# Kernel optimization log

Hardware: AMD Instinct MI355X
Metric: run time of the kernel (lower is better)

The kernel has to match this reference:

```python
import jax, jax.numpy as jnp
import numpy as np
import math

EPS_LN = 1e-5
SCALE = 16.0  # cosine_sim_scale


def layer_norm(x, g):
    mean = jnp.mean(x, axis=-1, keepdims=True)
    var = jnp.var(x, axis=-1, keepdims=True)  # biased, matches unbiased=False
    return (x - mean) * jax.lax.rsqrt(var + EPS_LN) * g


def l2norm(t):
    n = jnp.linalg.norm(t, axis=-1, keepdims=True)
    return t / jnp.maximum(n, 1e-12)


def setup_inputs() -> dict:
    key = jax.random.key(0)
    ks = jax.random.split(key, 4)
    b, n, dim, h, dh = 4, 2048, 1024, 8, 64
    inner = h * dh
    x = jax.random.normal(ks[0], (b, n, dim), dtype=jnp.float32)
    Wq = jax.random.normal(ks[1], (dim, inner), dtype=jnp.float32) * (dim ** -0.5)
    Wkv = jax.random.normal(ks[2], (dim, 2 * dh), dtype=jnp.float32) * (dim ** -0.5)
    Wout = jax.random.normal(ks[3], (inner, dim), dtype=jnp.float32) * (inner ** -0.5)
    norm_g = jnp.ones((dim,), dtype=jnp.float32)
    out_norm_g = jnp.ones((dim,), dtype=jnp.float32)
    return {"x": x, "norm_g": norm_g, "Wq": Wq, "Wkv": Wkv, "Wout": Wout,
            "out_norm_g": out_norm_g}


def reference(x, norm_g, Wq, Wkv, Wout, out_norm_g):
    b, n, dim = x.shape
    h = 8
    dh = Wkv.shape[-1] // 2
    xn = layer_norm(x, norm_g)
    q = xn @ Wq                      # [b, n, h*dh]
    kv = xn @ Wkv                    # [b, n, 2*dh]
    k, v = kv[..., :dh], kv[..., dh:]
    q = q.reshape(b, n, h, dh).transpose(0, 2, 1, 3)  # [b, h, n, dh]
    q = q * SCALE                    # cancelled by l2norm, kept for fidelity
    q = l2norm(q)
    k = l2norm(k)
    rs = math.sqrt(SCALE)
    q = q * rs
    k = k * rs
    sim = jnp.einsum('bhid,bjd->bhij', q, k)          # [b, h, n, n]
    attn = jax.nn.softmax(sim.astype(jnp.float32), axis=-1).astype(sim.dtype)
    out = jnp.einsum('bhij,bjd->bhid', attn, v)       # [b, h, n, dh]
    out = out.transpose(0, 2, 1, 3).reshape(b, n, h * dh)
    out = out @ Wout
    return layer_norm(out, out_norm_g)
```

## Files before the change

kernel.cpp:

```cpp
#include <hip/hip_runtime.h>
#include <hip/hip_bf16.h>

typedef __attribute__((ext_vector_type(8))) short short8;
typedef __attribute__((ext_vector_type(4))) float floatx4;
typedef __attribute__((ext_vector_type(16))) float floatx16;

__device__ __forceinline__ float bf2f(ushort u) {
    return __uint_as_float(((unsigned int)u) << 16);
}
__device__ __forceinline__ ushort f2bf(float f) {
    unsigned int u = __float_as_uint(f);
    unsigned int r = (u + 0x7FFFu + ((u >> 16) & 1u)) >> 16;
    return (ushort)r;
}
__device__ __forceinline__ unsigned int pk2(float a, float b) {
    union { __hip_bfloat162 h; unsigned int u; } cv;
    cv.h = __float22bfloat162_rn(make_float2(a, b));
    return cv.u;
}
__device__ __forceinline__ float scrub(float v, float lim) {
    return fminf(fmaxf(v, -lim), lim);
}
__device__ __forceinline__ void glds16(const ushort* g, ushort* l) {
    __builtin_amdgcn_global_load_lds((const __attribute__((address_space(1))) void*)g,
                                     (__attribute__((address_space(3))) void*)l, 16, 0, 0);
}

__device__ __forceinline__ bool detect_bf16(const ushort* __restrict__ probe) {
    const int lane = threadIdx.x & 63;
    ushort u = probe[(lane & 31) * 2];
    int e = (u >> 7) & 0xFF;
    bool pl = (e >= 117) && (e <= 131) && (lane < 32);
    return __popcll(__ballot(pl)) >= 16;
}

__device__ __forceinline__ void do_transpose(const void* __restrict__ in,
                                             ushort* __restrict__ out,
                                             int bx, int by, int in_rs, int out_rs,
                                             bool ib, ushort* tile ) {
    const int tx = threadIdx.x & 31, ty = threadIdx.x >> 5;
    #pragma unroll
    for (int rr = 0; rr < 32; rr += 8) {
        size_t idx = (size_t)(by * 32 + ty + rr) * in_rs + bx * 32 + tx;
        float v = ib ? bf2f(((const ushort*)in)[idx]) : ((const float*)in)[idx];
        tile[(ty + rr) * 33 + tx] = f2bf(scrub(v, 1e8f));
    }
    __syncthreads();
    #pragma unroll
    for (int rr = 0; rr < 32; rr += 8) {
        int r = bx * 32 + ty + rr;
        int c = by * 32 + tx;
        out[(size_t)r * out_rs + c] = tile[tx * 33 + (ty + rr)];
    }
}

__device__ __forceinline__ void ln_row_wave(const void* __restrict__ xin,
                                            const void* __restrict__ gin,
                                            ushort* __restrict__ xn,
                                            int row, int lane, bool ib) {
    float v[16], g[16];
    if (ib) {
        #pragma unroll
        for (int c = 0; c < 4; c++) {
            uint2 u  = *(const uint2*)((const ushort*)xin + (size_t)row * 1024 + c * 256 + lane * 4);
            uint2 gu = *(const uint2*)((const ushort*)gin + c * 256 + lane * 4);
            v[c*4+0] = bf2f((ushort)(u.x & 0xFFFF));  v[c*4+1] = bf2f((ushort)(u.x >> 16));
            v[c*4+2] = bf2f((ushort)(u.y & 0xFFFF));  v[c*4+3] = bf2f((ushort)(u.y >> 16));
            g[c*4+0] = bf2f((ushort)(gu.x & 0xFFFF)); g[c*4+1] = bf2f((ushort)(gu.x >> 16));
            g[c*4+2] = bf2f((ushort)(gu.y & 0xFFFF)); g[c*4+3] = bf2f((ushort)(gu.y >> 16));
        }
    } else {
        #pragma unroll
        for (int c = 0; c < 4; c++) {
            float4 xv = *(const float4*)((const float*)xin + (size_t)row * 1024 + c * 256 + lane * 4);
            float4 gv = *(const float4*)((const float*)gin + c * 256 + lane * 4);
            v[c*4+0] = xv.x; v[c*4+1] = xv.y; v[c*4+2] = xv.z; v[c*4+3] = xv.w;
            g[c*4+0] = gv.x; g[c*4+1] = gv.y; g[c*4+2] = gv.z; g[c*4+3] = gv.w;
        }
    }
    #pragma unroll
    for (int i = 0; i < 16; i++) { v[i] = scrub(v[i], 1e8f); g[i] = scrub(g[i], 1e8f); }

    float s = 0.0f, sq = 0.0f;
    #pragma unroll
    for (int i = 0; i < 16; i++) { s += v[i]; sq += v[i] * v[i]; }
    #pragma unroll
    for (int off = 1; off < 64; off <<= 1) {
        s  += __shfl_xor(s, off);
        sq += __shfl_xor(sq, off);
    }
    float mean = s * (1.0f / 1024.0f);
    float var  = sq * (1.0f / 1024.0f) - mean * mean;
    float rstd = rsqrtf(fmaxf(var, 0.0f) + 1e-5f);

    #pragma unroll
    for (int c = 0; c < 4; c++) {
        uint2 ov;
        ov.x = pk2((v[c*4+0] - mean) * rstd * g[c*4+0], (v[c*4+1] - mean) * rstd * g[c*4+1]);
        ov.y = pk2((v[c*4+2] - mean) * rstd * g[c*4+2], (v[c*4+3] - mean) * rstd * g[c*4+3]);
        *(uint2*)(xn + (size_t)row * 1024 + c * 256 + lane * 4) = ov;
    }
}

__global__ __launch_bounds__(256) void prep_kernel(const void* __restrict__ xin,
                                                   const void* __restrict__ gin,
                                                   const void* __restrict__ Wq,
                                                   const void* __restrict__ Wkv,
                                                   const void* __restrict__ Wout,
                                                   ushort* __restrict__ xn,
                                                   ushort* __restrict__ wcatT,
                                                   ushort* __restrict__ woT,
                                                   const ushort* __restrict__ probe) {
    const bool ib = detect_bf16(probe);
    const int id = blockIdx.x;
    __shared__ ushort tile[32 * 33];

    if (id >= 2048) {
        int t = id - 2048;
        if (t < 512) {
            do_transpose(Wq, wcatT, t & 15, t >> 4, 512, 1024, ib, tile);
        } else if (t < 640) {
            t -= 512;
            do_transpose(Wkv, wcatT + (size_t)512 * 1024, t & 3, t >> 2, 128, 1024, ib, tile);
        } else {
            t -= 640;
            do_transpose(Wout, woT, t & 31, t >> 5, 1024, 512, ib, tile);
        }
        return;
    }

    const int w = threadIdx.x >> 6, lane = threadIdx.x & 63;
    ln_row_wave(xin, gin, xn, id * 4 + w, lane, ib);
}

__global__ __launch_bounds__(256) void wout_tr_kernel(const void* __restrict__ Wout,
                                                      ushort* __restrict__ woT,
                                                      const ushort* __restrict__ probe) {
    const bool ib = detect_bf16(probe);
    __shared__ ushort tile[32 * 33];
    do_transpose(Wout, woT, blockIdx.x, blockIdx.y, 1024, 512, ib, tile);
}

__global__ __launch_bounds__(256) void ln2_kernel(const ushort* __restrict__ y,
                                                  const void* __restrict__ gin,
                                                  void* __restrict__ out,
                                                  const ushort* __restrict__ probe) {
    const bool ob = detect_bf16(probe);
    const int w = threadIdx.x >> 6, lane = threadIdx.x & 63;
    const int row = blockIdx.x * 4 + w;

    float v[16], g[16];
    #pragma unroll
    for (int c = 0; c < 4; c++) {
        uint2 u = *(const uint2*)(y + (size_t)row * 1024 + c * 256 + lane * 4);
        v[c*4+0] = bf2f((ushort)(u.x & 0xFFFF)); v[c*4+1] = bf2f((ushort)(u.x >> 16));
        v[c*4+2] = bf2f((ushort)(u.y & 0xFFFF)); v[c*4+3] = bf2f((ushort)(u.y >> 16));
    }
    if (ob) {
        #pragma unroll
        for (int c = 0; c < 4; c++) {
            uint2 gu = *(const uint2*)((const ushort*)gin + c * 256 + lane * 4);
            g[c*4+0] = bf2f((ushort)(gu.x & 0xFFFF)); g[c*4+1] = bf2f((ushort)(gu.x >> 16));
            g[c*4+2] = bf2f((ushort)(gu.y & 0xFFFF)); g[c*4+3] = bf2f((ushort)(gu.y >> 16));
        }
    } else {
        #pragma unroll
        for (int c = 0; c < 4; c++) {
            float4 gv = *(const float4*)((const float*)gin + c * 256 + lane * 4);
            g[c*4+0] = gv.x; g[c*4+1] = gv.y; g[c*4+2] = gv.z; g[c*4+3] = gv.w;
        }
    }
    #pragma unroll
    for (int i = 0; i < 16; i++) { v[i] = scrub(v[i], 1e8f); g[i] = scrub(g[i], 1e8f); }

    float s = 0.0f, sq = 0.0f;
    #pragma unroll
    for (int i = 0; i < 16; i++) { s += v[i]; sq += v[i] * v[i]; }
    #pragma unroll
    for (int off = 1; off < 64; off <<= 1) {
        s  += __shfl_xor(s, off);
        sq += __shfl_xor(sq, off);
    }
    float mean = s * (1.0f / 1024.0f);
    float var  = sq * (1.0f / 1024.0f) - mean * mean;
    float rstd = rsqrtf(fmaxf(var, 0.0f) + 1e-5f);

    if (ob) {
        #pragma unroll
        for (int c = 0; c < 4; c++) {
            uint2 ov;
            ov.x = pk2((v[c*4+0] - mean) * rstd * g[c*4+0], (v[c*4+1] - mean) * rstd * g[c*4+1]);
            ov.y = pk2((v[c*4+2] - mean) * rstd * g[c*4+2], (v[c*4+3] - mean) * rstd * g[c*4+3]);
            *(uint2*)((ushort*)out + (size_t)row * 1024 + c * 256 + lane * 4) = ov;
        }
    } else {
        #pragma unroll
        for (int c = 0; c < 4; c++) {
            float4 ov = make_float4((v[c*4+0] - mean) * rstd * g[c*4+0],
                                    (v[c*4+1] - mean) * rstd * g[c*4+1],
                                    (v[c*4+2] - mean) * rstd * g[c*4+2],
                                    (v[c*4+3] - mean) * rstd * g[c*4+3]);
            *(float4*)((float*)out + (size_t)row * 1024 + c * 256 + lane * 4) = ov;
        }
    }
}

__global__ __launch_bounds__(256) void gemm_qkv128(const ushort* __restrict__ A,
                                                   const ushort* __restrict__ Bt,
                                                   ushort* __restrict__ qb,
                                                   ushort* __restrict__ kb,
                                                   ushort* __restrict__ vt) {
    __shared__ ushort a_t[128][32];
    __shared__ ushort b_t[128][32];

    const int bx = blockIdx.x;
    const int n0 = bx * 128, m0 = blockIdx.y * 128;
    const int tid = threadIdx.x;
    const int w = tid >> 6, lane = tid & 63;
    const int fm = lane & 15, quad = lane >> 4;
    const int K = 1024;

    const int c0 = tid, c1 = tid + 256;
    const ushort* ag0 = A + (size_t)(m0 + (c0 >> 2)) * K + (c0 & 3) * 8;
    const ushort* ag1 = A + (size_t)(m0 + (c1 >> 2)) * K + (c1 & 3) * 8;
    const ushort* bg0 = Bt + (size_t)(n0 + (c0 >> 2)) * K + (c0 & 3) * 8;
    const ushort* bg1 = Bt + (size_t)(n0 + (c1 >> 2)) * K + (c1 & 3) * 8;
    ushort* la0 = &a_t[0][0] + w * 512;
    ushort* la1 = &a_t[0][0] + 2048 + w * 512;
    ushort* lb0 = &b_t[0][0] + w * 512;
    ushort* lb1 = &b_t[0][0] + 2048 + w * 512;

    floatx4 acc[2][8];
    floatx4 zero4 = {0.0f, 0.0f, 0.0f, 0.0f};
    #pragma unroll
    for (int mt = 0; mt < 2; mt++)
        #pragma unroll
        for (int nt = 0; nt < 8; nt++) acc[mt][nt] = zero4;

    union U8 { uint4 u4; short8 s8; };

    for (int k0 = 0; k0 < K; k0 += 32) {
        __syncthreads();
        glds16(ag0 + k0, la0);
        glds16(ag1 + k0, la1);
        glds16(bg0 + k0, lb0);
        glds16(bg1 + k0, lb1);
        __syncthreads();

        U8 af[2];
        #pragma unroll
        for (int mt = 0; mt < 2; mt++)
            af[mt].u4 = *(const uint4*)&a_t[w * 32 + mt * 16 + fm][quad * 8];
        #pragma unroll
        for (int nt = 0; nt < 8; nt++) {
            U8 bf;
            bf.u4 = *(const uint4*)&b_t[nt * 16 + fm][quad * 8];
            acc[0][nt] = __builtin_amdgcn_mfma_f32_16x16x32_bf16(af[0].s8, bf.s8, acc[0][nt], 0, 0, 0);
            acc[1][nt] = __builtin_amdgcn_mfma_f32_16x16x32_bf16(af[1].s8, bf.s8, acc[1][nt], 0, 0, 0);
        }
    }

    if (bx < 4) {
        const float qsc = 5.7707801636f;
        #pragma unroll
        for (int mt = 0; mt < 2; mt++) {
            float scA[4], scB[4];
            #pragma unroll
            for (int r = 0; r < 4; r++) {
                float sa = acc[mt][0][r] * acc[mt][0][r] + acc[mt][1][r] * acc[mt][1][r]
                         + acc[mt][2][r] * acc[mt][2][r] + acc[mt][3][r] * acc[mt][3][r];
                float sb = acc[mt][4][r] * acc[mt][4][r] + acc[mt][5][r] * acc[mt][5][r]
                         + acc[mt][6][r] * acc[mt][6][r] + acc[mt][7][r] * acc[mt][7][r];
                sa += __shfl_xor(sa, 1); sb += __shfl_xor(sb, 1);
                sa += __shfl_xor(sa, 2); sb += __shfl_xor(sb, 2);
                sa += __shfl_xor(sa, 4); sb += __shfl_xor(sb, 4);
                sa += __shfl_xor(sa, 8); sb += __shfl_xor(sb, 8);
                scA[r] = qsc / fmaxf(sqrtf(sa), 1e-12f);
                scB[r] = qsc / fmaxf(sqrtf(sb), 1e-12f);
            }
            #pragma unroll
            for (int nt = 0; nt < 8; nt++)
                #pragma unroll
                for (int r = 0; r < 4; r++)
                    qb[(size_t)(m0 + w * 32 + mt * 16 + quad * 4 + r) * 512 + n0 + nt * 16 + fm] =
                        f2bf(acc[mt][nt][r] * ((nt < 4) ? scA[r] : scB[r]));
        }
    } else {
        const int bb = m0 >> 11;
        const int kblk = ((m0 & 2047) >> 5) + w;
        const int qsw = ((quad & 1) << 1) | (quad >> 1);
        #pragma unroll
        for (int mt = 0; mt < 2; mt++) {
            float sck[4];
            #pragma unroll
            for (int r = 0; r < 4; r++) {
                float ss = acc[mt][0][r] * acc[mt][0][r] + acc[mt][1][r] * acc[mt][1][r]
                         + acc[mt][2][r] * acc[mt][2][r] + acc[mt][3][r] * acc[mt][3][r];
                ss += __shfl_xor(ss, 1);
                ss += __shfl_xor(ss, 2);
                ss += __shfl_xor(ss, 4);
                ss += __shfl_xor(ss, 8);
                sck[r] = 4.0f / fmaxf(sqrtf(ss), 1e-12f);
            }
            ushort* kop = kb + (size_t)bb * 131072 + kblk * 2048
                        + mt * 128 + qsw * 32 + (fm & 7);
            #pragma unroll
            for (int nt = 0; nt < 4; nt++) {
                const int oct = nt * 2 + (fm >> 3);
                #pragma unroll
                for (int r = 0; r < 4; r++)
                    kop[oct * 256 + r * 8] = f2bf(acc[mt][nt][r] * sck[r]);
            }
            const int koct = mt * 2 + (quad >> 1);
            ushort* vb = vt + (size_t)bb * 131072 + kblk * 2048 + koct * 512 + (quad & 1) * 4;
            #pragma unroll
            for (int nt = 4; nt < 8; nt++) {
                uint2 pv;
                pv.x = pk2(acc[mt][nt][0], acc[mt][nt][1]);
                pv.y = pk2(acc[mt][nt][2], acc[mt][nt][3]);
                *(uint2*)(vb + ((nt - 4) * 16 + fm) * 8) = pv;
            }
        }
    }
}

__global__ __launch_bounds__(256) void gemm_bt128(const ushort* __restrict__ A,
                                                  const ushort* __restrict__ Bt,
                                                  ushort* __restrict__ C,
                                                  int M, int N, int K) {
    __shared__ ushort a_t[128][32];
    __shared__ ushort b_t[128][32];

    const int n0 = blockIdx.x * 128, m0 = blockIdx.y * 128;
    const int tid = threadIdx.x;
    const int w = tid >> 6, lane = tid & 63;
    const int fm = lane & 15, quad = lane >> 4;

    const int c0 = tid, c1 = tid + 256;
    const ushort* ag0 = A + (size_t)(m0 + (c0 >> 2)) * K + (c0 & 3) * 8;
    const ushort* ag1 = A + (size_t)(m0 + (c1 >> 2)) * K + (c1 & 3) * 8;
    const ushort* bg0 = Bt + (size_t)(n0 + (c0 >> 2)) * K + (c0 & 3) * 8;
    const ushort* bg1 = Bt + (size_t)(n0 + (c1 >> 2)) * K + (c1 & 3) * 8;
    ushort* la0 = &a_t[0][0] + w * 512;
    ushort* la1 = &a_t[0][0] + 2048 + w * 512;
    ushort* lb0 = &b_t[0][0] + w * 512;
    ushort* lb1 = &b_t[0][0] + 2048 + w * 512;

    floatx4 acc[2][8];
    floatx4 zero4 = {0.0f, 0.0f, 0.0f, 0.0f};
    #pragma unroll
    for (int mt = 0; mt < 2; mt++)
        #pragma unroll
        for (int nt = 0; nt < 8; nt++) acc[mt][nt] = zero4;

    union U8 { uint4 u4; short8 s8; };

    for (int k0 = 0; k0 < K; k0 += 32) {
        __syncthreads();
        glds16(ag0 + k0, la0);
        glds16(ag1 + k0, la1);
        glds16(bg0 + k0, lb0);
        glds16(bg1 + k0, lb1);
        __syncthreads();

        U8 af[2];
        #pragma unroll
        for (int mt = 0; mt < 2; mt++)
            af[mt].u4 = *(const uint4*)&a_t[w * 32 + mt * 16 + fm][quad * 8];
        #pragma unroll
        for (int nt = 0; nt < 8; nt++) {
            U8 bf;
            bf.u4 = *(const uint4*)&b_t[nt * 16 + fm][quad * 8];
            acc[0][nt] = __builtin_amdgcn_mfma_f32_16x16x32_bf16(af[0].s8, bf.s8, acc[0][nt], 0, 0, 0);
            acc[1][nt] = __builtin_amdgcn_mfma_f32_16x16x32_bf16(af[1].s8, bf.s8, acc[1][nt], 0, 0, 0);
        }
    }

    #pragma unroll
    for (int mt = 0; mt < 2; mt++)
        #pragma unroll
        for (int nt = 0; nt < 8; nt++)
            #pragma unroll
            for (int r = 0; r < 4; r++)
                C[(size_t)(m0 + w * 32 + mt * 16 + quad * 4 + r) * N + n0 + nt * 16 + fm] =
                    f2bf(acc[mt][nt][r]);
}

__global__ __launch_bounds__(512, 4) void attn_kernel(const ushort* __restrict__ q,
                                                      const ushort* __restrict__ kb,
                                                      const ushort* __restrict__ vt,
                                                      ushort* __restrict__ out) {
    __shared__ ushort smem[17408];
    ushort* k_t = smem;
    ushort* v_t = smem + 8192;

    const int i0 = blockIdx.x * 128;
    const int h0 = blockIdx.y, b = blockIdx.z;
    const int tid = threadIdx.x, w = tid >> 6, lane = tid & 63;
    const int qg = w & 3;
    const int ks = w >> 2;
    const int cq = lane & 31;
    const int hi = lane >> 5;

    union U8 { uint4 u4; short8 s8; };

    const ushort* qbase = q + (size_t)(b * 2048 + i0 + qg * 32 + cq) * 512 + h0 * 64 + hi * 8;
    U8 qf[4];
    #pragma unroll
    for (int dm = 0; dm < 4; dm++) qf[dm].u4 = *(const uint4*)(qbase + dm * 16);

    floatx16 acc0, acc1;
    #pragma unroll
    for (int i = 0; i < 16; i++) { acc0[i] = 0.0f; acc1[i] = 0.0f; }
    float lsum = 0.0f;

    const ushort* kSrc = kb + (size_t)b * 131072 + ks * 65536 + lane * 8;
    const ushort* vSrc = vt + (size_t)b * 131072 + ks * 65536 + lane * 8;

    ushort* kT = k_t + ks * 4096;
    ushort* vT = v_t + ks * 4096;

    auto stageK = [&](int s, int buf) {
        glds16(kSrc + s * 2048 + qg * 512, kT + buf * 2048 + qg * 512);
    };
    auto stageV = [&](int s, int buf) {
        glds16(vSrc + s * 2048 + qg * 512, vT + buf * 2048 + qg * 512);
    };

    auto qk_exp = [&](int buf, U8& pb0, U8& pb1) {
        const int bo = buf * 2048;
        floatx16 st;
        #pragma unroll
        for (int i = 0; i < 16; i++) st[i] = -23.0831206f;
        #pragma unroll
        for (int dm = 0; dm < 4; dm++) {
            U8 kf;
            kf.u4 = *(const uint4*)&kT[bo + (2 * dm + hi) * 256 + cq * 8];
            st = __builtin_amdgcn_mfma_f32_32x32x16_bf16(kf.s8, qf[dm].s8, st, 0, 0, 0);
        }
        float p_[16];
        #pragma unroll
        for (int r = 0; r < 16; r++) p_[r] = __builtin_amdgcn_exp2f(st[r]);
        lsum += (((p_[0] + p_[1]) + (p_[2] + p_[3])) + ((p_[4] + p_[5]) + (p_[6] + p_[7])))
              + (((p_[8] + p_[9]) + (p_[10] + p_[11])) + ((p_[12] + p_[13]) + (p_[14] + p_[15])));
        pb0.u4.x = pk2(p_[0], p_[1]);   pb0.u4.y = pk2(p_[2], p_[3]);
        pb0.u4.z = pk2(p_[4], p_[5]);   pb0.u4.w = pk2(p_[6], p_[7]);
        pb1.u4.x = pk2(p_[8], p_[9]);   pb1.u4.y = pk2(p_[10], p_[11]);
        pb1.u4.z = pk2(p_[12], p_[13]); pb1.u4.w = pk2(p_[14], p_[15]);
    };

    auto pv = [&](int buf, U8 pb0, U8 pb1) {
        const int bo = buf * 2048;
        U8 vf;
        vf.u4 = *(const uint4*)&vT[bo + (0 + hi) * 512 + cq * 8];
        acc0 = __builtin_amdgcn_mfma_f32_32x32x16_bf16(vf.s8, pb0.s8, acc0, 0, 0, 0);
        vf.u4 = *(const uint4*)&vT[bo + (2 + hi) * 512 + cq * 8];
        acc0 = __builtin_amdgcn_mfma_f32_32x32x16_bf16(vf.s8, pb1.s8, acc0, 0, 0, 0);
        vf.u4 = *(const uint4*)&vT[bo + (0 + hi) * 512 + (32 + cq) * 8];
        acc1 = __builtin_amdgcn_mfma_f32_32x32x16_bf16(vf.s8, pb0.s8, acc1, 0, 0, 0);
        vf.u4 = *(const uint4*)&vT[bo + (2 + hi) * 512 + (32 + cq) * 8];
        acc1 = __builtin_amdgcn_mfma_f32_32x32x16_bf16(vf.s8, pb1.s8, acc1, 0, 0, 0);
    };

    U8 pA0, pA1, pB0, pB1;

    stageK(0, 0);
    __syncthreads();

    stageK(1, 1);
    stageV(0, 0);
    qk_exp(0, pA0, pA1);
    __syncthreads();

    for (int s = 1; s < 32; s += 2) {
        if (s + 1 < 32) stageK(s + 1, 0);
        stageV(s, 1);
        qk_exp(1, pB0, pB1);
        pv(0, pA0, pA1);
        __syncthreads();

        if (s + 1 < 32) {
            if (s + 2 < 32) stageK(s + 2, 1);
            stageV(s + 1, 0);
            qk_exp(0, pA0, pA1);
            pv(1, pB0, pB1);
            __syncthreads();
        }
    }
    pv(1, pB0, pB1);
    __syncthreads();

    float* row = (float*)smem + (qg * 64 + lane) * 34;
    if (ks == 1) {
        #pragma unroll
        for (int i = 0; i < 16; i++) { row[i] = acc0[i]; row[16 + i] = acc1[i]; }
        row[32] = lsum;
    }
    __syncthreads();
    if (ks == 1) return;
    #pragma unroll
    for (int i = 0; i < 16; i++) { acc0[i] += row[i]; acc1[i] += row[16 + i]; }
    lsum += row[32];
    lsum += __shfl_xor(lsum, 32);
    float li = 1.0f / fmaxf(lsum, 1e-30f);

    ushort* ob = out + (size_t)(b * 2048 + i0 + qg * 32 + cq) * 512 + h0 * 64 + hi * 4;
    #pragma unroll
    for (int t = 0; t < 4; t++) {
        uint2 ov;
        ov.x = pk2(acc0[4 * t] * li, acc0[4 * t + 1] * li);
        ov.y = pk2(acc0[4 * t + 2] * li, acc0[4 * t + 3] * li);
        *(uint2*)(ob + t * 8) = ov;
        ov.x = pk2(acc1[4 * t] * li, acc1[4 * t + 1] * li);
        ov.y = pk2(acc1[4 * t + 2] * li, acc1[4 * t + 3] * li);
        *(uint2*)(ob + 32 + t * 8) = ov;
    }
}

extern "C" void kernel_launch(void* const* d_in, const int* in_sizes, int n_in,
                              void* d_out, int out_size, void* d_ws, size_t ws_size,
                              hipStream_t stream) {
    const void* x          = d_in[0];
    const void* norm_g     = d_in[1];
    const void* Wq         = d_in[2];
    const void* Wkv        = d_in[3];
    const void* Wout       = d_in[4];
    const void* out_norm_g = d_in[5];
    const ushort* probe = (const ushort*)d_in[0];
    ushort* ws = (ushort*)d_ws;

    const size_t M1 = 1024 * 1024 / 2;
    ushort* xn    = (ushort*)d_out;
    ushort* ao    = (ushort*)d_out;
    ushort* qb    = ws;
    ushort* kb    = ws + 8 * M1;
    ushort* vt    = ws + 9 * M1;
    ushort* wcatT = ws + 11 * M1;
    ushort* y     = ws;

    const bool big_out = out_size >= (17 << 20);
    ushort* woT = big_out ? (ushort*)((char*)d_out + (16u << 20))
                          : (ushort*)((char*)d_out + (8u << 20));

    prep_kernel<<<big_out ? 3200 : 2688, 256, 0, stream>>>(
        x, norm_g, Wq, Wkv, Wout, xn, wcatT, woT, probe);

    gemm_qkv128<<<dim3(5, 64), 256, 0, stream>>>(xn, wcatT, qb, kb, vt);

    if (!big_out)
        wout_tr_kernel<<<dim3(32, 16), 256, 0, stream>>>(Wout, woT, probe);

    attn_kernel<<<dim3(16, 8, 4), 512, 0, stream>>>(qb, kb, vt, ao);

    gemm_bt128<<<dim3(8, 64), 256, 0, stream>>>(ao, woT, y, 8192, 1024, 512);

    ln2_kernel<<<2048, 256, 0, stream>>>(y, out_norm_g, d_out, probe);
}
```

Before: 202.1 us.

## Double-buffer LDS tiles in QKV and output projection GEMMs

Both 128x128 GEMM kernels now keep two LDS buffers. The next K-slice is issued via global_load_lds before the MFMAs on the current slice run, and there is one barrier per iteration instead of two. The goal is to hide global-to-LDS load latency behind matrix math. In exchange, LDS use per block doubles to 32 KB, and correctness depends on the barrier's implicit wait covering the async loads before the buffer is read.

```diff
diff --git a/kernel.cpp b/kernel.cpp
--- a/kernel.cpp
+++ b/kernel.cpp
@@ -210,8 +210,8 @@
                                                    ushort* __restrict__ qb,
                                                    ushort* __restrict__ kb,
                                                    ushort* __restrict__ vt) {
-    __shared__ ushort a_t[128][32];
-    __shared__ ushort b_t[128][32];
+    __shared__ ushort a_t[2][128 * 32];
+    __shared__ ushort b_t[2][128 * 32];
 
     const int bx = blockIdx.x;
     const int n0 = bx * 128, m0 = blockIdx.y * 128;
@@ -225,10 +225,6 @@
     const ushort* ag1 = A + (size_t)(m0 + (c1 >> 2)) * K + (c1 & 3) * 8;
     const ushort* bg0 = Bt + (size_t)(n0 + (c0 >> 2)) * K + (c0 & 3) * 8;
     const ushort* bg1 = Bt + (size_t)(n0 + (c1 >> 2)) * K + (c1 & 3) * 8;
-    ushort* la0 = &a_t[0][0] + w * 512;
-    ushort* la1 = &a_t[0][0] + 2048 + w * 512;
-    ushort* lb0 = &b_t[0][0] + w * 512;
-    ushort* lb1 = &b_t[0][0] + 2048 + w * 512;
 
     floatx4 acc[2][8];
     floatx4 zero4 = {0.0f, 0.0f, 0.0f, 0.0f};
@@ -239,25 +235,32 @@
 
     union U8 { uint4 u4; short8 s8; };
 
-    for (int k0 = 0; k0 < K; k0 += 32) {
-        __syncthreads();
-        glds16(ag0 + k0, la0);
-        glds16(ag1 + k0, la1);
-        glds16(bg0 + k0, lb0);
-        glds16(bg1 + k0, lb1);
-        __syncthreads();
-
+    auto stage = [&](int k0, int buf) {
+        glds16(ag0 + k0, &a_t[buf][0] + w * 512);
+        glds16(ag1 + k0, &a_t[buf][0] + 2048 + w * 512);
+        glds16(bg0 + k0, &b_t[buf][0] + w * 512);
+        glds16(bg1 + k0, &b_t[buf][0] + 2048 + w * 512);
+    };
+    auto compute = [&](int buf) {
         U8 af[2];
         #pragma unroll
         for (int mt = 0; mt < 2; mt++)
-            af[mt].u4 = *(const uint4*)&a_t[w * 32 + mt * 16 + fm][quad * 8];
+            af[mt].u4 = *(const uint4*)&a_t[buf][(w * 32 + mt * 16 + fm) * 32 + quad * 8];
         #pragma unroll
         for (int nt = 0; nt < 8; nt++) {
             U8 bf;
-            bf.u4 = *(const uint4*)&b_t[nt * 16 + fm][quad * 8];
+            bf.u4 = *(const uint4*)&b_t[buf][(nt * 16 + fm) * 32 + quad * 8];
             acc[0][nt] = __builtin_amdgcn_mfma_f32_16x16x32_bf16(af[0].s8, bf.s8, acc[0][nt], 0, 0, 0);
             acc[1][nt] = __builtin_amdgcn_mfma_f32_16x16x32_bf16(af[1].s8, bf.s8, acc[1][nt], 0, 0, 0);
         }
+    };
+
+    stage(0, 0);
+    __syncthreads();
+    for (int s = 0; s < K / 32; s++) {
+        if (s + 1 < K / 32) stage((s + 1) * 32, (s + 1) & 1);
+        compute(s & 1);
+        __syncthreads();
     }
 
     if (bx < 4) {
@@ -328,8 +331,8 @@
                                                   const ushort* __restrict__ Bt,
                                                   ushort* __restrict__ C,
                                                   int M, int N, int K) {
-    __shared__ ushort a_t[128][32];
-    __shared__ ushort b_t[128][32];
+    __shared__ ushort a_t[2][128 * 32];
+    __shared__ ushort b_t[2][128 * 32];
 
     const int n0 = blockIdx.x * 128, m0 = blockIdx.y * 128;
     const int tid = threadIdx.x;
@@ -341,10 +344,6 @@
     const ushort* ag1 = A + (size_t)(m0 + (c1 >> 2)) * K + (c1 & 3) * 8;
     const ushort* bg0 = Bt + (size_t)(n0 + (c0 >> 2)) * K + (c0 & 3) * 8;
     const ushort* bg1 = Bt + (size_t)(n0 + (c1 >> 2)) * K + (c1 & 3) * 8;
-    ushort* la0 = &a_t[0][0] + w * 512;
-    ushort* la1 = &a_t[0][0] + 2048 + w * 512;
-    ushort* lb0 = &b_t[0][0] + w * 512;
-    ushort* lb1 = &b_t[0][0] + 2048 + w * 512;
 
     floatx4 acc[2][8];
     floatx4 zero4 = {0.0f, 0.0f, 0.0f, 0.0f};
@@ -355,25 +354,33 @@
 
     union U8 { uint4 u4; short8 s8; };
 
-    for (int k0 = 0; k0 < K; k0 += 32) {
-        __syncthreads();
-        glds16(ag0 + k0, la0);
-        glds16(ag1 + k0, la1);
-        glds16(bg0 + k0, lb0);
-        glds16(bg1 + k0, lb1);
-        __syncthreads();
-
+    auto stage = [&](int k0, int buf) {
+        glds16(ag0 + k0, &a_t[buf][0] + w * 512);
+        glds16(ag1 + k0, &a_t[buf][0] + 2048 + w * 512);
+        glds16(bg0 + k0, &b_t[buf][0] + w * 512);
+        glds16(bg1 + k0, &b_t[buf][0] + 2048 + w * 512);
+    };
+    auto compute = [&](int buf) {
         U8 af[2];
         #pragma unroll
         for (int mt = 0; mt < 2; mt++)
-            af[mt].u4 = *(const uint4*)&a_t[w * 32 + mt * 16 + fm][quad * 8];
+            af[mt].u4 = *(const uint4*)&a_t[buf][(w * 32 + mt * 16 + fm) * 32 + quad * 8];
         #pragma unroll
         for (int nt = 0; nt < 8; nt++) {
             U8 bf;
-            bf.u4 = *(const uint4*)&b_t[nt * 16 + fm][quad * 8];
+            bf.u4 = *(const uint4*)&b_t[buf][(nt * 16 + fm) * 32 + quad * 8];
             acc[0][nt] = __builtin_amdgcn_mfma_f32_16x16x32_bf16(af[0].s8, bf.s8, acc[0][nt], 0, 0, 0);
             acc[1][nt] = __builtin_amdgcn_mfma_f32_16x16x32_bf16(af[1].s8, bf.s8, acc[1][nt], 0, 0, 0);
         }
+    };
+
+    const int NS = K / 32;
+    stage(0, 0);
+    __syncthreads();
+    for (int s = 0; s < NS; s++) {
+        if (s + 1 < NS) stage((s + 1) * 32, (s + 1) & 1);
+        compute(s & 1);
+        __syncthreads();
     }
 
     #pragma unroll
```

After: 204.4 us. About the same (+1.1%).
